# Optimization experiments

Measured on AMD Instinct MI355X. Metric: run time of the kernel, lower is better.

Reference implementation:

```python
import jax, jax.numpy as jnp
import numpy as np

B, S, T, V, D = 256, 256, 256, 512, 512


def _gru_cell(x, h, Wih, Whh, bih, bhh):
    # torch GRU semantics: gates ordered [r, z, n]
    gi = x @ Wih.T + bih            # [B, 3D]
    gh = h @ Whh.T + bhh            # [B, 3D]
    gi_r, gi_z, gi_n = jnp.split(gi, 3, axis=-1)
    gh_r, gh_z, gh_n = jnp.split(gh, 3, axis=-1)
    r = jax.nn.sigmoid(gi_r + gh_r)
    z = jax.nn.sigmoid(gi_z + gh_z)
    n = jnp.tanh(gi_n + r * gh_n)
    return (1.0 - z) * n + z * h


def setup_inputs() -> dict:
    key = jax.random.key(0)
    ks = jax.random.split(key, 14)
    s = 0.05
    inp = {
        "src": jax.random.randint(ks[0], (B, S), 0, V),
        "trg": jax.random.randint(ks[1], (B, T), 0, V),
        "src_mask": jnp.ones((B, S), dtype=bool),
        "trg_mask": jnp.ones((B, T), dtype=bool),
        "enc_emb": jax.random.normal(ks[2], (V, D), jnp.float32) * s,
        "enc_Wih": jax.random.normal(ks[3], (3 * D, D), jnp.float32) * s,
        "enc_Whh": jax.random.normal(ks[4], (3 * D, D), jnp.float32) * s,
        "enc_bih": jnp.zeros((3 * D,), jnp.float32),
        "enc_bhh": jnp.zeros((3 * D,), jnp.float32),
        "dec_emb": jax.random.normal(ks[5], (V, D), jnp.float32) * s,
        "dec_Wih": jax.random.normal(ks[6], (3 * D, D), jnp.float32) * s,
        "dec_Whh": jax.random.normal(ks[7], (3 * D, D), jnp.float32) * s,
        "dec_bih": jnp.zeros((3 * D,), jnp.float32),
        "dec_bhh": jnp.zeros((3 * D,), jnp.float32),
        "out_W": jax.random.normal(ks[8], (V, D), jnp.float32) * s,
        "out_b": jnp.zeros((V,), jnp.float32),
    }
    return inp


def reference(src, trg, src_mask, trg_mask,
              enc_emb, enc_Wih, enc_Whh, enc_bih, enc_bhh,
              dec_emb, dec_Wih, dec_Whh, dec_bih, dec_bhh,
              out_W, out_b):
    b = src.shape[0]
    d = enc_Whh.shape[1]

    # ---- encoder: embed (eval: no dropout) + GRU over src ----
    enc_x = enc_emb[src]                       # [B, S, D]
    h0 = jnp.zeros((b, d), enc_emb.dtype)

    def enc_step(h, x):
        return _gru_cell(x, h, enc_Wih, enc_Whh, enc_bih, enc_bhh), None

    h_enc, _ = jax.lax.scan(enc_step, h0, jnp.swapaxes(enc_x, 0, 1))

    # ---- decoder: relu(embed) + GRU step + linear per timestep ----
    dec_x = jax.nn.relu(dec_emb[trg])          # [B, T, D]

    def dec_step(h, x):
        h = _gru_cell(x, h, dec_Wih, dec_Whh, dec_bih, dec_bhh)
        logits = h @ out_W.T + out_b           # [B, V]
        return h, logits

    _, logits = jax.lax.scan(dec_step, h_enc, jnp.swapaxes(dec_x, 0, 1))
    logits = jnp.swapaxes(logits, 0, 1)        # [B, T, V]
    return jax.nn.log_softmax(logits, axis=-1)
```

## Files before the change

kernel.cpp:

```cpp
#include <hip/hip_runtime.h>
#include <cstdint>
#include <cstddef>

namespace {
constexpr int Dh = 512;
constexpr int G3 = 1536;
constexpr int NB = 256;
constexpr int SL = 256;
constexpr int TL = 256;
constexpr int NV = 512;
}

typedef __attribute__((ext_vector_type(8))) short bf16x8;
typedef __attribute__((ext_vector_type(4))) float f32x4;

__device__ __forceinline__ unsigned short f2bf(float f) {
  unsigned int u = __float_as_uint(f);
  u = (u + 0x7FFFu + ((u >> 16) & 1u)) >> 16;
  return (unsigned short)u;
}
__device__ __forceinline__ float bf2f(unsigned short s) {
  return __uint_as_float(((unsigned int)s) << 16);
}


__global__ __launch_bounds__(256) void cvt_bf16(const float* __restrict__ in,
                                                unsigned short* __restrict__ out,
                                                int n4, int relu) {
  int i = blockIdx.x * 256 + threadIdx.x;
  if (i >= n4) return;
  float4 v = ((const float4*)in)[i];
  if (relu) {
    v.x = fmaxf(v.x, 0.f); v.y = fmaxf(v.y, 0.f);
    v.z = fmaxf(v.z, 0.f); v.w = fmaxf(v.w, 0.f);
  }
  ushort4 o;
  o.x = f2bf(v.x); o.y = f2bf(v.y); o.z = f2bf(v.z); o.w = f2bf(v.w);
  ((ushort4*)out)[i] = o;
}

__global__ __launch_bounds__(256) void pack_whh(const unsigned short* __restrict__ Wb,
                                                unsigned short* __restrict__ Wpk) {
  const int idx = blockIdx.x * 256 + threadIdx.x;
  if (idx >= 16 * 6 * 16 * 64) return;
  const int dt = idx / 6144;
  const int rem = idx - dt * 6144;
  const int slot = rem >> 10;
  const int kk = (rem >> 6) & 15;
  const int l = rem & 63;
  const int n = slot / 3, g = slot - n * 3;
  const int row = g * 512 + dt * 32 + n * 16 + (l & 15);
  const int k = kk * 32 + (l >> 4) * 8;
  *(uint4*)(Wpk + (size_t)idx * 8) = *(const uint4*)(Wb + (size_t)row * Dh + k);
}

template <int AMODE, int OMODE>
__global__ __launch_bounds__(256) void gemm_bf16(
    const unsigned short* __restrict__ Abase, const int* __restrict__ idx,
    const unsigned short* __restrict__ W, const float* __restrict__ bias,
    void* __restrict__ Cout, int N) {
  __shared__ unsigned short lds_a[8 * 128 * 8];
  __shared__ unsigned short lds_b[8 * 128 * 8];
  const int t = threadIdx.x;
  const int n0 = blockIdx.x * 128;
  const int m0 = blockIdx.y * 128;
  const int w = t >> 6, l = t & 63;
  const int mq = (w & 1) * 64, nq = (w >> 1) * 64;
  const int l15 = l & 15, lh = l >> 4;

  const int sm = t & 127;
  const int sk = (t >> 7) * 4;
  const unsigned short* arow;
  if (AMODE == 0) {
    arow = Abase + (size_t)idx[m0 + sm] * Dh;
  } else {
    int row = m0 + sm;
    arow = Abase + ((size_t)(row & 255) * NB + (row >> 8)) * Dh;
  }
  const unsigned short* brow = W + (size_t)(n0 + sm) * Dh;

  f32x4 acc[4][4];
#pragma unroll
  for (int i = 0; i < 4; ++i)
#pragma unroll
    for (int j = 0; j < 4; ++j) acc[i][j] = (f32x4)0.f;

  for (int k0 = 0; k0 < Dh; k0 += 64) {
    __syncthreads();
#pragma unroll
    for (int i = 0; i < 4; ++i) {
      int kc = sk + i;
      *(uint4*)&lds_a[(kc * 128 + sm) * 8] = *(const uint4*)(arow + k0 + kc * 8);
      *(uint4*)&lds_b[(kc * 128 + sm) * 8] = *(const uint4*)(brow + k0 + kc * 8);
    }
    __syncthreads();
#pragma unroll
    for (int q = 0; q < 2; ++q) {
      bf16x8 af[4], bfr[4];
#pragma unroll
      for (int i = 0; i < 4; ++i)
        af[i] = *(const bf16x8*)&lds_a[((q * 4 + lh) * 128 + mq + i * 16 + l15) * 8];
#pragma unroll
      for (int j = 0; j < 4; ++j)
        bfr[j] = *(const bf16x8*)&lds_b[((q * 4 + lh) * 128 + nq + j * 16 + l15) * 8];
#pragma unroll
      for (int i = 0; i < 4; ++i)
#pragma unroll
        for (int j = 0; j < 4; ++j)
          acc[i][j] = __builtin_amdgcn_mfma_f32_16x16x32_bf16(af[i], bfr[j], acc[i][j], 0, 0, 0);
    }
  }

#pragma unroll
  for (int j = 0; j < 4; ++j) {
    const int col = n0 + nq + j * 16 + l15;
    const float bv = bias[col];
#pragma unroll
    for (int i = 0; i < 4; ++i) {
#pragma unroll
      for (int r = 0; r < 4; ++r) {
        const int row = m0 + mq + i * 16 + lh * 4 + r;
        const float v = acc[i][j][r] + bv;
        if (OMODE == 0) {
          ((float*)Cout)[(size_t)row * N + col] = v;
        } else {
          const int b = row >> 8, s = row & 255;
          const int g = col >> 9, d = col & 511;
          const int dt = d >> 5, nn_ = (d >> 4) & 1, cl = d & 15;
          ((unsigned short*)Cout)[((((size_t)s * NB + b) * 16 + dt) * 16 + cl) * 8 + nn_ * 3 + g] = f2bf(v);
        }
      }
    }
  }
}

__global__ __launch_bounds__(64, 1) void gru_step3(
    const unsigned short* __restrict__ Wpk,
    const unsigned short* __restrict__ gi,
    const float* __restrict__ bhh,
    const float* __restrict__ h32_in, float* __restrict__ h32_out,
    const unsigned short* __restrict__ hb_in, unsigned short* __restrict__ hb_out,
    int s) {
  const int wt = blockIdx.x;
  const int b0 = (wt >> 4) * 16;
  const int dt = wt & 15, d0 = dt * 32;
  const int l = threadIdx.x & 63, l15 = l & 15, lh = l >> 4;

  bf16x8 af[16];
#pragma unroll
  for (int kk = 0; kk < 16; ++kk)
    af[kk] = *(const bf16x8*)(hb_in + (size_t)(b0 + l15) * Dh + kk * 32 + lh * 8);

  uint4 gpr[4];
#pragma unroll
  for (int r = 0; r < 4; ++r)
    gpr[r] = *(const uint4*)(gi + ((((size_t)s * NB + b0 + lh * 4 + r) * 16 + dt) * 16 + l15) * 8);

  float hp[2][4];
#pragma unroll
  for (int n = 0; n < 2; ++n)
#pragma unroll
    for (int r = 0; r < 4; ++r)
      hp[n][r] = h32_in[(size_t)(b0 + lh * 4 + r) * Dh + d0 + n * 16 + l15];

  f32x4 acc[2][3];
#pragma unroll
  for (int n = 0; n < 2; ++n)
#pragma unroll
    for (int g = 0; g < 3; ++g) acc[n][g] = (f32x4)0.f;

  const unsigned short* wb = Wpk + ((size_t)dt * 6144 + l) * 8;
#pragma unroll
  for (int n = 0; n < 2; ++n)
#pragma unroll
    for (int g = 0; g < 3; ++g) {
      const int slot = n * 3 + g;
      bf16x8 bv[16];
#pragma unroll
      for (int kk = 0; kk < 16; ++kk)
        bv[kk] = *(const bf16x8*)(wb + (size_t)(slot * 16 + kk) * 64 * 8);
#pragma unroll
      for (int kk = 0; kk < 16; ++kk)
        acc[n][g] = __builtin_amdgcn_mfma_f32_16x16x32_bf16(af[kk], bv[kk], acc[n][g], 0, 0, 0);
    }

#pragma unroll
  for (int n = 0; n < 2; ++n) {
    const int d = d0 + n * 16 + l15;
    const float br = bhh[d], bz = bhh[512 + d], bn = bhh[1024 + d];
#pragma unroll
    for (int r = 0; r < 4; ++r) {
      const unsigned short* gp = (const unsigned short*)&gpr[r];
      const float gir = bf2f(gp[n * 3 + 0]);
      const float giz = bf2f(gp[n * 3 + 1]);
      const float gin = bf2f(gp[n * 3 + 2]);
      const float rr = 1.f / (1.f + __expf(-(gir + acc[n][0][r] + br)));
      const float zz = 1.f / (1.f + __expf(-(giz + acc[n][1][r] + bz)));
      const float x2 = gin + rr * (acc[n][2][r] + bn);
      const float nn = 1.f - 2.f / (__expf(2.f * x2) + 1.f);
      const float o = (1.f - zz) * nn + zz * hp[n][r];
      const int b = b0 + lh * 4 + r;
      h32_out[(size_t)b * Dh + d] = o;
      hb_out[(size_t)b * Dh + d] = f2bf(o);
    }
  }
}

__global__ __launch_bounds__(256) void logsoftmax512(float* __restrict__ x) {
  const int row = blockIdx.x * 4 + (threadIdx.x >> 6);
  const int lane = threadIdx.x & 63;
  float* p = x + (size_t)row * NV + lane * 8;
  float4 v0 = *(const float4*)p;
  float4 v1 = *(const float4*)(p + 4);
  float m = fmaxf(fmaxf(fmaxf(v0.x, v0.y), fmaxf(v0.z, v0.w)),
                  fmaxf(fmaxf(v1.x, v1.y), fmaxf(v1.z, v1.w)));
#pragma unroll
  for (int o = 1; o < 64; o <<= 1) m = fmaxf(m, __shfl_xor(m, o, 64));
  float s = expf(v0.x - m) + expf(v0.y - m) + expf(v0.z - m) + expf(v0.w - m) +
            expf(v1.x - m) + expf(v1.y - m) + expf(v1.z - m) + expf(v1.w - m);
#pragma unroll
  for (int o = 1; o < 64; o <<= 1) s += __shfl_xor(s, o, 64);
  const float ls = m + logf(s);
  v0.x -= ls; v0.y -= ls; v0.z -= ls; v0.w -= ls;
  v1.x -= ls; v1.y -= ls; v1.z -= ls; v1.w -= ls;
  *(float4*)p = v0;
  *(float4*)(p + 4) = v1;
}

extern "C" void kernel_launch(void* const* d_in, const int* in_sizes, int n_in,
                              void* d_out, int out_size, void* d_ws, size_t ws_size,
                              hipStream_t stream) {
  (void)in_sizes; (void)n_in; (void)out_size; (void)ws_size;
  const int* src = (const int*)d_in[0];
  const int* trg = (const int*)d_in[1];
  const float* enc_emb = (const float*)d_in[4];
  const float* enc_Wih = (const float*)d_in[5];
  const float* enc_Whh = (const float*)d_in[6];
  const float* enc_bih = (const float*)d_in[7];
  const float* enc_bhh = (const float*)d_in[8];
  const float* dec_emb = (const float*)d_in[9];
  const float* dec_Wih = (const float*)d_in[10];
  const float* dec_Whh = (const float*)d_in[11];
  const float* dec_bih = (const float*)d_in[12];
  const float* dec_bhh = (const float*)d_in[13];
  const float* out_W = (const float*)d_in[14];
  const float* out_b = (const float*)d_in[15];

  char* ws = (char*)d_ws;
  size_t off = 0;
  auto alloc = [&](size_t bytes) -> char* {
    char* p = ws + off;
    off += (bytes + 255) & ~(size_t)255;
    return p;
  };
  typedef unsigned short u16;
  u16* gi = (u16*)alloc((size_t)NB * SL * 16 * 16 * 8 * 2);
  u16* hb_all = (u16*)alloc((size_t)TL * NB * Dh * 2);
  float* h32a = (float*)alloc((size_t)NB * Dh * 4);
  float* h32b = (float*)alloc((size_t)NB * Dh * 4);
  u16* hb0 = (u16*)alloc((size_t)NB * Dh * 2);
  u16* hb1 = (u16*)alloc((size_t)NB * Dh * 2);
  u16* embB_e = (u16*)alloc((size_t)NV * Dh * 2);
  u16* embB_d = (u16*)alloc((size_t)NV * Dh * 2);
  u16* WihB_e = (u16*)alloc((size_t)G3 * Dh * 2);
  u16* WhhB_e = (u16*)alloc((size_t)G3 * Dh * 2);
  u16* WihB_d = (u16*)alloc((size_t)G3 * Dh * 2);
  u16* WhhB_d = (u16*)alloc((size_t)G3 * Dh * 2);
  u16* outWB = (u16*)alloc((size_t)NV * Dh * 2);
  u16* Wpk_e = (u16*)alloc((size_t)16 * 6 * 16 * 64 * 8 * 2);
  u16* Wpk_d = (u16*)alloc((size_t)16 * 6 * 16 * 64 * 8 * 2);

  cvt_bf16<<<(NV * Dh / 4 + 255) / 256, 256, 0, stream>>>(enc_emb, embB_e, NV * Dh / 4, 0);
  cvt_bf16<<<(NV * Dh / 4 + 255) / 256, 256, 0, stream>>>(dec_emb, embB_d, NV * Dh / 4, 1);
  cvt_bf16<<<(G3 * Dh / 4 + 255) / 256, 256, 0, stream>>>(enc_Wih, WihB_e, G3 * Dh / 4, 0);
  cvt_bf16<<<(G3 * Dh / 4 + 255) / 256, 256, 0, stream>>>(enc_Whh, WhhB_e, G3 * Dh / 4, 0);
  cvt_bf16<<<(G3 * Dh / 4 + 255) / 256, 256, 0, stream>>>(dec_Wih, WihB_d, G3 * Dh / 4, 0);
  cvt_bf16<<<(G3 * Dh / 4 + 255) / 256, 256, 0, stream>>>(dec_Whh, WhhB_d, G3 * Dh / 4, 0);
  cvt_bf16<<<(NV * Dh / 4 + 255) / 256, 256, 0, stream>>>(out_W, outWB, NV * Dh / 4, 0);
  pack_whh<<<384, 256, 0, stream>>>(WhhB_e, Wpk_e);
  pack_whh<<<384, 256, 0, stream>>>(WhhB_d, Wpk_d);
  hipMemsetAsync(h32a, 0, (size_t)NB * Dh * 4, stream);
  hipMemsetAsync(hb0, 0, (size_t)NB * Dh * 2, stream);

  dim3 ggi(G3 / 128, NB * SL / 128);
  gemm_bf16<0, 2><<<ggi, 256, 0, stream>>>(embB_e, src, WihB_e, enc_bih, gi, G3);

  for (int s = 0; s < SL; ++s) {
    const float* i32 = (s & 1) ? h32b : h32a;
    float* o32 = (s & 1) ? h32a : h32b;
    const u16* ib = (s & 1) ? hb1 : hb0;
    u16* ob = (s & 1) ? hb0 : hb1;
    gru_step3<<<dim3(256), 64, 0, stream>>>(Wpk_e, gi, enc_bhh, i32, o32, ib, ob, s);
  }

  gemm_bf16<0, 2><<<ggi, 256, 0, stream>>>(embB_d, trg, WihB_d, dec_bih, gi, G3);

  for (int s = 0; s < TL; ++s) {
    const float* i32 = (s & 1) ? h32b : h32a;
    float* o32 = (s & 1) ? h32a : h32b;
    const u16* ib = (s == 0) ? hb0 : (hb_all + (size_t)(s - 1) * NB * Dh);
    u16* ob = hb_all + (size_t)s * NB * Dh;
    gru_step3<<<dim3(256), 64, 0, stream>>>(Wpk_d, gi, dec_bhh, i32, o32, ib, ob, s);
  }

  dim3 glg(NV / 128, NB * TL / 128);
  gemm_bf16<1, 0><<<glg, 256, 0, stream>>>(hb_all, nullptr, outWB, out_b, d_out, NV);
  logsoftmax512<<<NB * TL / 4, 256, 0, stream>>>((float*)d_out);
}
```

Before: 3.939 ms.

## Replace per-timestep GRU launches with persistent kernel using flag-based sync

```diff
diff --git a/kernel.cpp b/kernel.cpp
--- a/kernel.cpp
+++ b/kernel.cpp
@@ -13,6 +13,7 @@
 
 typedef __attribute__((ext_vector_type(8))) short bf16x8;
 typedef __attribute__((ext_vector_type(4))) float f32x4;
+typedef unsigned long long u64t;
 
 __device__ __forceinline__ unsigned short f2bf(float f) {
   unsigned int u = __float_as_uint(f);
@@ -134,75 +135,141 @@
   }
 }
 
-__global__ __launch_bounds__(64, 1) void gru_step3(
+__global__ __launch_bounds__(64, 1) void gru_persist2(
     const unsigned short* __restrict__ Wpk,
     const unsigned short* __restrict__ gi,
     const float* __restrict__ bhh,
-    const float* __restrict__ h32_in, float* __restrict__ h32_out,
-    const unsigned short* __restrict__ hb_in, unsigned short* __restrict__ hb_out,
-    int s) {
+    const float* __restrict__ h32_init,
+    float* __restrict__ h32_final,
+    unsigned short* __restrict__ hbA,
+    unsigned short* __restrict__ hbB,
+    unsigned short* __restrict__ hb_all,
+    unsigned int* __restrict__ flags,
+    int nsteps) {
+  __shared__ unsigned short wl[6 * 16 * 64 * 8];
   const int wt = blockIdx.x;
   const int b0 = (wt >> 4) * 16;
   const int dt = wt & 15, d0 = dt * 32;
-  const int l = threadIdx.x & 63, l15 = l & 15, lh = l >> 4;
-
-  bf16x8 af[16];
-#pragma unroll
-  for (int kk = 0; kk < 16; ++kk)
-    af[kk] = *(const bf16x8*)(hb_in + (size_t)(b0 + l15) * Dh + kk * 32 + lh * 8);
-
-  uint4 gpr[4];
-#pragma unroll
-  for (int r = 0; r < 4; ++r)
-    gpr[r] = *(const uint4*)(gi + ((((size_t)s * NB + b0 + lh * 4 + r) * 16 + dt) * 16 + l15) * 8);
-
-  float hp[2][4];
-#pragma unroll
-  for (int n = 0; n < 2; ++n)
-#pragma unroll
-    for (int r = 0; r < 4; ++r)
-      hp[n][r] = h32_in[(size_t)(b0 + lh * 4 + r) * Dh + d0 + n * 16 + l15];
-
-  f32x4 acc[2][3];
-#pragma unroll
-  for (int n = 0; n < 2; ++n)
-#pragma unroll
-    for (int g = 0; g < 3; ++g) acc[n][g] = (f32x4)0.f;
-
-  const unsigned short* wb = Wpk + ((size_t)dt * 6144 + l) * 8;
-#pragma unroll
-  for (int n = 0; n < 2; ++n)
-#pragma unroll
-    for (int g = 0; g < 3; ++g) {
-      const int slot = n * 3 + g;
-      bf16x8 bv[16];
-#pragma unroll
-      for (int kk = 0; kk < 16; ++kk)
-        bv[kk] = *(const bf16x8*)(wb + (size_t)(slot * 16 + kk) * 64 * 8);
-#pragma unroll
-      for (int kk = 0; kk < 16; ++kk)
-        acc[n][g] = __builtin_amdgcn_mfma_f32_16x16x32_bf16(af[kk], bv[kk], acc[n][g], 0, 0, 0);
-    }
-
+  const int l = threadIdx.x;
+  const int l15 = l & 15, lh = l >> 4;
+
+  {
+    const uint4* wsrc = (const uint4*)(Wpk + (size_t)dt * 49152);
+    uint4* wdst = (uint4*)wl;
+#pragma unroll 4
+    for (int i = 0; i < 96; ++i) wdst[i * 64 + l] = wsrc[i * 64 + l];
+  }
+  __syncthreads();
+
+  float br_[2], bz_[2], bn_[2];
 #pragma unroll
   for (int n = 0; n < 2; ++n) {
     const int d = d0 + n * 16 + l15;
-    const float br = bhh[d], bz = bhh[512 + d], bn = bhh[1024 + d];
-#pragma unroll
-    for (int r = 0; r < 4; ++r) {
-      const unsigned short* gp = (const unsigned short*)&gpr[r];
-      const float gir = bf2f(gp[n * 3 + 0]);
-      const float giz = bf2f(gp[n * 3 + 1]);
-      const float gin = bf2f(gp[n * 3 + 2]);
-      const float rr = 1.f / (1.f + __expf(-(gir + acc[n][0][r] + br)));
-      const float zz = 1.f / (1.f + __expf(-(giz + acc[n][1][r] + bz)));
-      const float x2 = gin + rr * (acc[n][2][r] + bn);
-      const float nn = 1.f - 2.f / (__expf(2.f * x2) + 1.f);
-      const float o = (1.f - zz) * nn + zz * hp[n][r];
-      const int b = b0 + lh * 4 + r;
-      h32_out[(size_t)b * Dh + d] = o;
-      hb_out[(size_t)b * Dh + d] = f2bf(o);
-    }
+    br_[n] = bhh[d]; bz_[n] = bhh[512 + d]; bn_[n] = bhh[1024 + d];
+  }
+
+  float hp[2][4];
+#pragma unroll
+  for (int n = 0; n < 2; ++n)
+#pragma unroll
+    for (int r = 0; r < 4; ++r)
+      hp[n][r] = h32_init ? h32_init[(size_t)(b0 + lh * 4 + r) * Dh + d0 + n * 16 + l15] : 0.f;
+
+  uint4 gpr[4];
+#pragma unroll
+  for (int r = 0; r < 4; ++r)
+    gpr[r] = *(const uint4*)(gi + ((((size_t)0 * NB + b0 + lh * 4 + r) * 16 + dt) * 16 + l15) * 8);
+
+  const unsigned int* fgrp = flags + (wt & ~15);
+
+  for (int s = 0; s < nsteps; ++s) {
+    const unsigned short* rdbuf;
+    unsigned short* wrbuf;
+    if (hb_all) {
+      rdbuf = (s == 0) ? hbA : hb_all + (size_t)(s - 1) * NB * Dh;
+      wrbuf = hb_all + (size_t)s * NB * Dh;
+    } else {
+      rdbuf = (s & 1) ? hbB : hbA;
+      wrbuf = (s & 1) ? hbA : hbB;
+    }
+
+    if (s > 0) {
+      const unsigned int tgt = (unsigned)s;
+      unsigned int f;
+      do {
+        f = __hip_atomic_load(fgrp + l15, __ATOMIC_RELAXED, __HIP_MEMORY_SCOPE_SYSTEM);
+        if (__all((int)(f >= tgt))) break;
+        __builtin_amdgcn_s_sleep(1);
+      } while (true);
+      asm volatile("" ::: "memory");
+    }
+
+    const u64t* ap = (const u64t*)(rdbuf + (size_t)(b0 + l15) * Dh + lh * 8);
+    bf16x8 af[16];
+#pragma unroll
+    for (int kk = 0; kk < 16; ++kk) {
+      union { u64t q[2]; bf16x8 v; } u;
+      u.q[0] = __hip_atomic_load(ap + kk * 8, __ATOMIC_RELAXED, __HIP_MEMORY_SCOPE_SYSTEM);
+      u.q[1] = __hip_atomic_load(ap + kk * 8 + 1, __ATOMIC_RELAXED, __HIP_MEMORY_SCOPE_SYSTEM);
+      af[kk] = u.v;
+    }
+
+    f32x4 acc[6];
+#pragma unroll
+    for (int sl_ = 0; sl_ < 6; ++sl_) acc[sl_] = (f32x4)0.f;
+#pragma unroll
+    for (int sl_ = 0; sl_ < 6; ++sl_)
+#pragma unroll
+      for (int kk = 0; kk < 16; ++kk) {
+        bf16x8 bv = *(const bf16x8*)&wl[((sl_ * 16 + kk) * 64 + l) * 8];
+        acc[sl_] = __builtin_amdgcn_mfma_f32_16x16x32_bf16(af[kk], bv, acc[sl_], 0, 0, 0);
+      }
+
+#pragma unroll
+    for (int n = 0; n < 2; ++n)
+#pragma unroll
+      for (int r = 0; r < 4; ++r) {
+        const unsigned short* gp = (const unsigned short*)&gpr[r];
+        const float gir = bf2f(gp[n * 3 + 0]);
+        const float giz = bf2f(gp[n * 3 + 1]);
+        const float gin = bf2f(gp[n * 3 + 2]);
+        const float rr = 1.f / (1.f + __expf(-(gir + acc[n * 3 + 0][r] + br_[n])));
+        const float zz = 1.f / (1.f + __expf(-(giz + acc[n * 3 + 1][r] + bz_[n])));
+        const float x2 = gin + rr * (acc[n * 3 + 2][r] + bn_[n]);
+        const float nn = 1.f - 2.f / (__expf(2.f * x2) + 1.f);
+        hp[n][r] = (1.f - zz) * nn + zz * hp[n][r];
+      }
+
+#pragma unroll
+    for (int n = 0; n < 2; ++n)
+#pragma unroll
+      for (int r = 0; r < 4; ++r) {
+        const float po = __shfl_xor(hp[n][r], 1, 64);
+        if ((l15 & 1) == 0) {
+          const unsigned int pk = (unsigned)f2bf(hp[n][r]) | ((unsigned)f2bf(po) << 16);
+          const int b = b0 + lh * 4 + r, d = d0 + n * 16 + l15;
+          __hip_atomic_store((unsigned int*)(wrbuf + (size_t)b * Dh + d), pk,
+                             __ATOMIC_RELAXED, __HIP_MEMORY_SCOPE_SYSTEM);
+        }
+      }
+
+    if (s + 1 < nsteps) {
+      asm volatile("s_waitcnt vmcnt(0)" ::: "memory");
+      if (l == 0)
+        __hip_atomic_store(flags + wt, (unsigned)(s + 1), __ATOMIC_RELAXED,
+                           __HIP_MEMORY_SCOPE_SYSTEM);
+#pragma unroll
+      for (int r = 0; r < 4; ++r)
+        gpr[r] = *(const uint4*)(gi + ((((size_t)(s + 1) * NB + b0 + lh * 4 + r) * 16 + dt) * 16 + l15) * 8);
+    }
+  }
+
+  if (h32_final) {
+#pragma unroll
+    for (int n = 0; n < 2; ++n)
+#pragma unroll
+      for (int r = 0; r < 4; ++r)
+        h32_final[(size_t)(b0 + lh * 4 + r) * Dh + d0 + n * 16 + l15] = hp[n][r];
   }
 }
 
@@ -256,10 +323,9 @@
   typedef unsigned short u16;
   u16* gi = (u16*)alloc((size_t)NB * SL * 16 * 16 * 8 * 2);
   u16* hb_all = (u16*)alloc((size_t)TL * NB * Dh * 2);
-  float* h32a = (float*)alloc((size_t)NB * Dh * 4);
-  float* h32b = (float*)alloc((size_t)NB * Dh * 4);
-  u16* hb0 = (u16*)alloc((size_t)NB * Dh * 2);
-  u16* hb1 = (u16*)alloc((size_t)NB * Dh * 2);
+  float* h_enc = (float*)alloc((size_t)NB * Dh * 4);
+  u16* hbA = (u16*)alloc((size_t)NB * Dh * 2);
+  u16* hbB = (u16*)alloc((size_t)NB * Dh * 2);
   u16* embB_e = (u16*)alloc((size_t)NV * Dh * 2);
   u16* embB_d = (u16*)alloc((size_t)NV * Dh * 2);
   u16* WihB_e = (u16*)alloc((size_t)G3 * Dh * 2);
@@ -269,6 +335,7 @@
   u16* outWB = (u16*)alloc((size_t)NV * Dh * 2);
   u16* Wpk_e = (u16*)alloc((size_t)16 * 6 * 16 * 64 * 8 * 2);
   u16* Wpk_d = (u16*)alloc((size_t)16 * 6 * 16 * 64 * 8 * 2);
+  unsigned int* flags = (unsigned int*)alloc(2 * 256 * 4);
 
   cvt_bf16<<<(NV * Dh / 4 + 255) / 256, 256, 0, stream>>>(enc_emb, embB_e, NV * Dh / 4, 0);
   cvt_bf16<<<(NV * Dh / 4 + 255) / 256, 256, 0, stream>>>(dec_emb, embB_d, NV * Dh / 4, 1);
@@ -279,29 +346,19 @@
   cvt_bf16<<<(NV * Dh / 4 + 255) / 256, 256, 0, stream>>>(out_W, outWB, NV * Dh / 4, 0);
   pack_whh<<<384, 256, 0, stream>>>(WhhB_e, Wpk_e);
   pack_whh<<<384, 256, 0, stream>>>(WhhB_d, Wpk_d);
-  hipMemsetAsync(h32a, 0, (size_t)NB * Dh * 4, stream);
-  hipMemsetAsync(hb0, 0, (size_t)NB * Dh * 2, stream);
+  hipMemsetAsync(hbA, 0, (size_t)NB * Dh * 2, stream);
+  hipMemsetAsync(flags, 0, 2 * 256 * 4, stream);
 
   dim3 ggi(G3 / 128, NB * SL / 128);
   gemm_bf16<0, 2><<<ggi, 256, 0, stream>>>(embB_e, src, WihB_e, enc_bih, gi, G3);
 
-  for (int s = 0; s < SL; ++s) {
-    const float* i32 = (s & 1) ? h32b : h32a;
-    float* o32 = (s & 1) ? h32a : h32b;
-    const u16* ib = (s & 1) ? hb1 : hb0;
-    u16* ob = (s & 1) ? hb0 : hb1;
-    gru_step3<<<dim3(256), 64, 0, stream>>>(Wpk_e, gi, enc_bhh, i32, o32, ib, ob, s);
-  }
+  gru_persist2<<<dim3(256), 64, 0, stream>>>(Wpk_e, gi, enc_bhh, nullptr, h_enc,
+                                             hbA, hbB, nullptr, flags, SL);
 
   gemm_bf16<0, 2><<<ggi, 256, 0, stream>>>(embB_d, trg, WihB_d, dec_bih, gi, G3);
 
-  for (int s = 0; s < TL; ++s) {
-    const float* i32 = (s & 1) ? h32b : h32a;
-    float* o32 = (s & 1) ? h32a : h32b;
-    const u16* ib = (s == 0) ? hb0 : (hb_all + (size_t)(s - 1) * NB * Dh);
-    u16* ob = hb_all + (size_t)s * NB * Dh;
-    gru_step3<<<dim3(256), 64, 0, stream>>>(Wpk_d, gi, dec_bhh, i32, o32, ib, ob, s);
-  }
+  gru_persist2<<<dim3(256), 64, 0, stream>>>(Wpk_d, gi, dec_bhh, h_enc, nullptr,
+                                             hbA, hbB, hb_all, flags + 256, TL);
 
   dim3 glg(NV / 128, NB * TL / 128);
   gemm_bf16<1, 0><<<glg, 256, 0, stream>>>(hb_all, nullptr, outWB, out_b, d_out, NV);
```

New measurement: 3.957 ms. Within noise of the previous version (+0.4%).

## Fuse output projection with log-softmax and merge weight conversion kernels

Applied to the files above, without the earlier changes.

```diff
diff --git a/kernel.cpp b/kernel.cpp
--- a/kernel.cpp
+++ b/kernel.cpp
@@ -24,25 +24,38 @@
 }
 
 
-__global__ __launch_bounds__(256) void cvt_bf16(const float* __restrict__ in,
-                                                unsigned short* __restrict__ out,
-                                                int n4, int relu) {
+__global__ __launch_bounds__(256) void cvt_all(
+    const float* __restrict__ a0, const float* __restrict__ a1,
+    const float* __restrict__ a2, const float* __restrict__ a3,
+    unsigned short* __restrict__ o0, unsigned short* __restrict__ o1,
+    unsigned short* __restrict__ o2, unsigned short* __restrict__ o3) {
   int i = blockIdx.x * 256 + threadIdx.x;
-  if (i >= n4) return;
-  float4 v = ((const float4*)in)[i];
-  if (relu) {
+  const float* src;
+  unsigned short* dst;
+  int base, rel = 0;
+  if (i < 65536) { src = a0; dst = o0; base = 0; }
+  else if (i < 131072) { src = a1; dst = o1; base = 65536; rel = 1; }
+  else if (i < 327680) { src = a2; dst = o2; base = 131072; }
+  else { src = a3; dst = o3; base = 327680; }
+  int j = i - base;
+  float4 v = ((const float4*)src)[j];
+  if (rel) {
     v.x = fmaxf(v.x, 0.f); v.y = fmaxf(v.y, 0.f);
     v.z = fmaxf(v.z, 0.f); v.w = fmaxf(v.w, 0.f);
   }
   ushort4 o;
   o.x = f2bf(v.x); o.y = f2bf(v.y); o.z = f2bf(v.z); o.w = f2bf(v.w);
-  ((ushort4*)out)[i] = o;
-}
-
-__global__ __launch_bounds__(256) void pack_whh(const unsigned short* __restrict__ Wb,
-                                                unsigned short* __restrict__ Wpk) {
-  const int idx = blockIdx.x * 256 + threadIdx.x;
-  if (idx >= 16 * 6 * 16 * 64) return;
+  ((ushort4*)dst)[j] = o;
+}
+
+__global__ __launch_bounds__(256) void pack_whh_f32(
+    const float* __restrict__ We, unsigned short* __restrict__ Pe,
+    const float* __restrict__ Wd, unsigned short* __restrict__ Pd) {
+  int idx = blockIdx.x * 256 + threadIdx.x;
+  if (idx >= 2 * 98304) return;
+  const float* Wb = (idx < 98304) ? We : Wd;
+  unsigned short* Wpk = (idx < 98304) ? Pe : Pd;
+  if (idx >= 98304) idx -= 98304;
   const int dt = idx / 6144;
   const int rem = idx - dt * 6144;
   const int slot = rem >> 10;
@@ -51,14 +64,33 @@
   const int n = slot / 3, g = slot - n * 3;
   const int row = g * 512 + dt * 32 + n * 16 + (l & 15);
   const int k = kk * 32 + (l >> 4) * 8;
-  *(uint4*)(Wpk + (size_t)idx * 8) = *(const uint4*)(Wb + (size_t)row * Dh + k);
-}
-
-template <int AMODE, int OMODE>
-__global__ __launch_bounds__(256) void gemm_bf16(
+  const float* s = Wb + (size_t)row * Dh + k;
+  unsigned short o[8];
+#pragma unroll
+  for (int j = 0; j < 8; ++j) o[j] = f2bf(s[j]);
+  *(uint4*)(Wpk + ((size_t)(idx < 0 ? 0 : 0) + (size_t)((dt * 6 + slot) * 16 + kk) * 64 + l) * 8) = *(uint4*)o;
+}
+
+__global__ __launch_bounds__(256) void pack_w16(const float* __restrict__ Wf,
+                                                unsigned short* __restrict__ Wpk) {
+  int idx = blockIdx.x * 256 + threadIdx.x;
+  if (idx >= 32 * 16 * 64) return;
+  const int nt = idx >> 10;
+  const int kk = (idx >> 6) & 15;
+  const int l = idx & 63;
+  const int row = nt * 16 + (l & 15);
+  const int k = kk * 32 + (l >> 4) * 8;
+  const float* s = Wf + (size_t)row * Dh + k;
+  unsigned short o[8];
+#pragma unroll
+  for (int j = 0; j < 8; ++j) o[j] = f2bf(s[j]);
+  *(uint4*)(Wpk + (size_t)idx * 8) = *(uint4*)o;
+}
+
+__global__ __launch_bounds__(256) void gemm_gi(
     const unsigned short* __restrict__ Abase, const int* __restrict__ idx,
     const unsigned short* __restrict__ W, const float* __restrict__ bias,
-    void* __restrict__ Cout, int N) {
+    unsigned short* __restrict__ Cout) {
   __shared__ unsigned short lds_a[8 * 128 * 8];
   __shared__ unsigned short lds_b[8 * 128 * 8];
   const int t = threadIdx.x;
@@ -70,13 +102,7 @@
 
   const int sm = t & 127;
   const int sk = (t >> 7) * 4;
-  const unsigned short* arow;
-  if (AMODE == 0) {
-    arow = Abase + (size_t)idx[m0 + sm] * Dh;
-  } else {
-    int row = m0 + sm;
-    arow = Abase + ((size_t)(row & 255) * NB + (row >> 8)) * Dh;
-  }
+  const unsigned short* arow = Abase + (size_t)idx[m0 + sm] * Dh;
   const unsigned short* brow = W + (size_t)(n0 + sm) * Dh;
 
   f32x4 acc[4][4];
@@ -121,30 +147,25 @@
       for (int r = 0; r < 4; ++r) {
         const int row = m0 + mq + i * 16 + lh * 4 + r;
         const float v = acc[i][j][r] + bv;
-        if (OMODE == 0) {
-          ((float*)Cout)[(size_t)row * N + col] = v;
-        } else {
-          const int b = row >> 8, s = row & 255;
-          const int g = col >> 9, d = col & 511;
-          const int dt = d >> 5, nn_ = (d >> 4) & 1, cl = d & 15;
-          ((unsigned short*)Cout)[((((size_t)s * NB + b) * 16 + dt) * 16 + cl) * 8 + nn_ * 3 + g] = f2bf(v);
-        }
+        const int b = row >> 8, s = row & 255;
+        const int g = col >> 9, d = col & 511;
+        const int dt = d >> 5, nn_ = (d >> 4) & 1, cl = d & 15;
+        Cout[((((size_t)s * NB + b) * 16 + dt) * 16 + cl) * 8 + nn_ * 3 + g] = f2bf(v);
       }
     }
   }
 }
 
-__global__ __launch_bounds__(64, 1) void gru_step3(
+__device__ __forceinline__ void gru_tile_body(
     const unsigned short* __restrict__ Wpk,
     const unsigned short* __restrict__ gi,
     const float* __restrict__ bhh,
     const float* __restrict__ h32_in, float* __restrict__ h32_out,
     const unsigned short* __restrict__ hb_in, unsigned short* __restrict__ hb_out,
-    int s) {
-  const int wt = blockIdx.x;
+    int s, int wt, int l) {
   const int b0 = (wt >> 4) * 16;
   const int dt = wt & 15, d0 = dt * 32;
-  const int l = threadIdx.x & 63, l15 = l & 15, lh = l >> 4;
+  const int l15 = l & 15, lh = l >> 4;
 
   bf16x8 af[16];
 #pragma unroll
@@ -206,25 +227,141 @@
   }
 }
 
-__global__ __launch_bounds__(256) void logsoftmax512(float* __restrict__ x) {
-  const int row = blockIdx.x * 4 + (threadIdx.x >> 6);
-  const int lane = threadIdx.x & 63;
-  float* p = x + (size_t)row * NV + lane * 8;
-  float4 v0 = *(const float4*)p;
-  float4 v1 = *(const float4*)(p + 4);
-  float m = fmaxf(fmaxf(fmaxf(v0.x, v0.y), fmaxf(v0.z, v0.w)),
-                  fmaxf(fmaxf(v1.x, v1.y), fmaxf(v1.z, v1.w)));
-#pragma unroll
-  for (int o = 1; o < 64; o <<= 1) m = fmaxf(m, __shfl_xor(m, o, 64));
-  float s = expf(v0.x - m) + expf(v0.y - m) + expf(v0.z - m) + expf(v0.w - m) +
-            expf(v1.x - m) + expf(v1.y - m) + expf(v1.z - m) + expf(v1.w - m);
-#pragma unroll
-  for (int o = 1; o < 64; o <<= 1) s += __shfl_xor(s, o, 64);
-  const float ls = m + logf(s);
-  v0.x -= ls; v0.y -= ls; v0.z -= ls; v0.w -= ls;
-  v1.x -= ls; v1.y -= ls; v1.z -= ls; v1.w -= ls;
-  *(float4*)p = v0;
-  *(float4*)(p + 4) = v1;
+__global__ __launch_bounds__(64, 1) void gru_step3(
+    const unsigned short* __restrict__ Wpk, const unsigned short* __restrict__ gi,
+    const float* __restrict__ bhh,
+    const float* __restrict__ h32_in, float* __restrict__ h32_out,
+    const unsigned short* __restrict__ hb_in, unsigned short* __restrict__ hb_out,
+    int s) {
+  gru_tile_body(Wpk, gi, bhh, h32_in, h32_out, hb_in, hb_out, s,
+                blockIdx.x, threadIdx.x & 63);
+}
+
+__global__ __launch_bounds__(256, 1) void gru_step4w(
+    const unsigned short* __restrict__ Wpk, const unsigned short* __restrict__ gi,
+    const float* __restrict__ bhh,
+    const float* __restrict__ h32_in, float* __restrict__ h32_out,
+    const unsigned short* __restrict__ hb_in, unsigned short* __restrict__ hb_out,
+    int s) {
+  gru_tile_body(Wpk, gi, bhh, h32_in, h32_out, hb_in, hb_out, s,
+                blockIdx.x * 4 + (threadIdx.x >> 6), threadIdx.x & 63);
+}
+
+__global__ __launch_bounds__(256, 1) void logits_ls(
+    const unsigned short* __restrict__ hb_all,
+    const unsigned short* __restrict__ Wpk,
+    const float* __restrict__ out_b,
+    float* __restrict__ out) {
+  __shared__ unsigned short Alds[64 * 32 * 8];
+  __shared__ float redm[4][32];
+  __shared__ float reds[4][32];
+  const int m0 = blockIdx.x * 32;
+  const int t = threadIdx.x;
+  const int w = t >> 6, l = t & 63;
+  const int l15 = l & 15, lh = l >> 4;
+
+#pragma unroll
+  for (int i = 0; i < 8; ++i) {
+    int id = i * 256 + t;
+    int row = id >> 6, kc = id & 63;
+    int orow = m0 + row;
+    int arow = (orow & 255) * NB + (orow >> 8);
+    *(uint4*)&Alds[(kc * 32 + row) * 8] = *(const uint4*)(hb_all + (size_t)arow * Dh + kc * 8);
+  }
+  __syncthreads();
+
+  bf16x8 af[2][16];
+#pragma unroll
+  for (int mi = 0; mi < 2; ++mi)
+#pragma unroll
+    for (int kk = 0; kk < 16; ++kk)
+      af[mi][kk] = *(const bf16x8*)&Alds[((kk * 4 + lh) * 32 + mi * 16 + l15) * 8];
+
+  f32x4 acc[2][8];
+#pragma unroll
+  for (int mi = 0; mi < 2; ++mi)
+#pragma unroll
+    for (int j = 0; j < 8; ++j) acc[mi][j] = (f32x4)0.f;
+
+#pragma unroll
+  for (int j = 0; j < 8; ++j) {
+    const int nt = w * 8 + j;
+    const unsigned short* bp = Wpk + ((size_t)(nt * 16) * 64 + l) * 8;
+    bf16x8 bv[16];
+#pragma unroll
+    for (int kk = 0; kk < 16; ++kk) bv[kk] = *(const bf16x8*)(bp + (size_t)kk * 64 * 8);
+#pragma unroll
+    for (int kk = 0; kk < 16; ++kk) {
+      acc[0][j] = __builtin_amdgcn_mfma_f32_16x16x32_bf16(af[0][kk], bv[kk], acc[0][j], 0, 0, 0);
+      acc[1][j] = __builtin_amdgcn_mfma_f32_16x16x32_bf16(af[1][kk], bv[kk], acc[1][j], 0, 0, 0);
+    }
+  }
+
+#pragma unroll
+  for (int j = 0; j < 8; ++j) {
+    const float bc = out_b[(w * 8 + j) * 16 + l15];
+#pragma unroll
+    for (int mi = 0; mi < 2; ++mi)
+#pragma unroll
+      for (int r = 0; r < 4; ++r) acc[mi][j][r] += bc;
+  }
+
+  float gmax[2][4];
+#pragma unroll
+  for (int mi = 0; mi < 2; ++mi)
+#pragma unroll
+    for (int r = 0; r < 4; ++r) {
+      float m = acc[mi][0][r];
+#pragma unroll
+      for (int j = 1; j < 8; ++j) m = fmaxf(m, acc[mi][j][r]);
+#pragma unroll
+      for (int off = 1; off < 16; off <<= 1) m = fmaxf(m, __shfl_xor(m, off, 16));
+      if (l15 == 0) redm[w][mi * 16 + lh * 4 + r] = m;
+      gmax[mi][r] = m;
+    }
+  __syncthreads();
+#pragma unroll
+  for (int mi = 0; mi < 2; ++mi)
+#pragma unroll
+    for (int r = 0; r < 4; ++r) {
+      const int row = mi * 16 + lh * 4 + r;
+      gmax[mi][r] = fmaxf(fmaxf(redm[0][row], redm[1][row]),
+                          fmaxf(redm[2][row], redm[3][row]));
+    }
+
+  float ls[2][4];
+#pragma unroll
+  for (int mi = 0; mi < 2; ++mi)
+#pragma unroll
+    for (int r = 0; r < 4; ++r) {
+      float sv = 0.f;
+#pragma unroll
+      for (int j = 0; j < 8; ++j) sv += expf(acc[mi][j][r] - gmax[mi][r]);
+#pragma unroll
+      for (int off = 1; off < 16; off <<= 1) sv += __shfl_xor(sv, off, 16);
+      if (l15 == 0) reds[w][mi * 16 + lh * 4 + r] = sv;
+    }
+  __syncthreads();
+#pragma unroll
+  for (int mi = 0; mi < 2; ++mi)
+#pragma unroll
+    for (int r = 0; r < 4; ++r) {
+      const int row = mi * 16 + lh * 4 + r;
+      const float tot = reds[0][row] + reds[1][row] + reds[2][row] + reds[3][row];
+      ls[mi][r] = gmax[mi][r] + logf(tot);
+    }
+
+#pragma unroll
+  for (int mi = 0; mi < 2; ++mi)
+#pragma unroll
+    for (int j = 0; j < 8; ++j) {
+      const int col = (w * 8 + j) * 16 + l15;
+#pragma unroll
+      for (int r = 0; r < 4; ++r) {
+        const size_t row = (size_t)m0 + mi * 16 + lh * 4 + r;
+        out[row * NV + col] = acc[mi][j][r] - ls[mi][r];
+      }
+    }
 }
 
 extern "C" void kernel_launch(void* const* d_in, const int* in_sizes, int n_in,
@@ -263,37 +400,30 @@
   u16* embB_e = (u16*)alloc((size_t)NV * Dh * 2);
   u16* embB_d = (u16*)alloc((size_t)NV * Dh * 2);
   u16* WihB_e = (u16*)alloc((size_t)G3 * Dh * 2);
-  u16* WhhB_e = (u16*)alloc((size_t)G3 * Dh * 2);
   u16* WihB_d = (u16*)alloc((size_t)G3 * Dh * 2);
-  u16* WhhB_d = (u16*)alloc((size_t)G3 * Dh * 2);
-  u16* outWB = (u16*)alloc((size_t)NV * Dh * 2);
   u16* Wpk_e = (u16*)alloc((size_t)16 * 6 * 16 * 64 * 8 * 2);
   u16* Wpk_d = (u16*)alloc((size_t)16 * 6 * 16 * 64 * 8 * 2);
-
-  cvt_bf16<<<(NV * Dh / 4 + 255) / 256, 256, 0, stream>>>(enc_emb, embB_e, NV * Dh / 4, 0);
-  cvt_bf16<<<(NV * Dh / 4 + 255) / 256, 256, 0, stream>>>(dec_emb, embB_d, NV * Dh / 4, 1);
-  cvt_bf16<<<(G3 * Dh / 4 + 255) / 256, 256, 0, stream>>>(enc_Wih, WihB_e, G3 * Dh / 4, 0);
-  cvt_bf16<<<(G3 * Dh / 4 + 255) / 256, 256, 0, stream>>>(enc_Whh, WhhB_e, G3 * Dh / 4, 0);
-  cvt_bf16<<<(G3 * Dh / 4 + 255) / 256, 256, 0, stream>>>(dec_Wih, WihB_d, G3 * Dh / 4, 0);
-  cvt_bf16<<<(G3 * Dh / 4 + 255) / 256, 256, 0, stream>>>(dec_Whh, WhhB_d, G3 * Dh / 4, 0);
-  cvt_bf16<<<(NV * Dh / 4 + 255) / 256, 256, 0, stream>>>(out_W, outWB, NV * Dh / 4, 0);
-  pack_whh<<<384, 256, 0, stream>>>(WhhB_e, Wpk_e);
-  pack_whh<<<384, 256, 0, stream>>>(WhhB_d, Wpk_d);
+  u16* outWpk = (u16*)alloc((size_t)32 * 16 * 64 * 8 * 2);
+
+  cvt_all<<<2048, 256, 0, stream>>>(enc_emb, dec_emb, enc_Wih, dec_Wih,
+                                    embB_e, embB_d, WihB_e, WihB_d);
+  pack_whh_f32<<<768, 256, 0, stream>>>(enc_Whh, Wpk_e, dec_Whh, Wpk_d);
+  pack_w16<<<128, 256, 0, stream>>>(out_W, outWpk);
   hipMemsetAsync(h32a, 0, (size_t)NB * Dh * 4, stream);
   hipMemsetAsync(hb0, 0, (size_t)NB * Dh * 2, stream);
 
   dim3 ggi(G3 / 128, NB * SL / 128);
-  gemm_bf16<0, 2><<<ggi, 256, 0, stream>>>(embB_e, src, WihB_e, enc_bih, gi, G3);
+  gemm_gi<<<ggi, 256, 0, stream>>>(embB_e, src, WihB_e, enc_bih, gi);
 
   for (int s = 0; s < SL; ++s) {
     const float* i32 = (s & 1) ? h32b : h32a;
     float* o32 = (s & 1) ? h32a : h32b;
     const u16* ib = (s & 1) ? hb1 : hb0;
     u16* ob = (s & 1) ? hb0 : hb1;
-    gru_step3<<<dim3(256), 64, 0, stream>>>(Wpk_e, gi, enc_bhh, i32, o32, ib, ob, s);
-  }
-
-  gemm_bf16<0, 2><<<ggi, 256, 0, stream>>>(embB_d, trg, WihB_d, dec_bih, gi, G3);
+    gru_step4w<<<dim3(64), 256, 0, stream>>>(Wpk_e, gi, enc_bhh, i32, o32, ib, ob, s);
+  }
+
+  gemm_gi<<<ggi, 256, 0, stream>>>(embB_d, trg, WihB_d, dec_bih, gi);
 
   for (int s = 0; s < TL; ++s) {
     const float* i32 = (s & 1) ? h32b : h32a;
@@ -303,7 +433,5 @@
     gru_step3<<<dim3(256), 64, 0, stream>>>(Wpk_d, gi, dec_bhh, i32, o32, ib, ob, s);
   }
 
-  dim3 glg(NV / 128, NB * TL / 128);
-  gemm_bf16<1, 0><<<glg, 256, 0, stream>>>(hb_all, nullptr, outWB, out_b, d_out, NV);
-  logsoftmax512<<<NB * TL / 4, 256, 0, stream>>>((float*)d_out);
-}
+  logits_ls<<<dim3(NB * TL / 32), 256, 0, stream>>>(hb_all, outWpk, out_b, (float*)d_out);
+}
```

After: 4.477 ms. 1.14x slower.
